# Optimization experiments

Measured on AMD Instinct MI355X. Metric: run time of the kernel, lower is better.

The kernel has to match this reference:

```python
import jax, jax.numpy as jnp
import numpy as np

N, E, IN, H, C = 50000, 800000, 128, 256, 2
EPS = 1e-5


def setup_inputs() -> dict:
    key = jax.random.key(0)
    ks = jax.random.split(key, 12)
    inp = {
        "x": jax.random.normal(ks[0], (N, IN), jnp.float32),
        "edge_index": jax.random.randint(ks[1], (2, E), 0, N, jnp.int32),
        "w_nei0": jax.random.normal(ks[2], (IN, H), jnp.float32) * 0.05,
        "w_root0": jax.random.normal(ks[3], (IN, H), jnp.float32) * 0.05,
        "b0": jnp.zeros((H,), jnp.float32),
        "w_nei": jax.random.normal(ks[4], (2, H, H), jnp.float32) * 0.05,
        "w_root": jax.random.normal(ks[5], (2, H, H), jnp.float32) * 0.05,
        "b": jnp.zeros((2, H), jnp.float32),
        "bn_gamma": jnp.ones((3, H), jnp.float32),
        "bn_beta": jnp.zeros((3, H), jnp.float32),
        "bn_mean": jax.random.normal(ks[6], (3, H), jnp.float32) * 0.05,
        "bn_var": jnp.ones((3, H), jnp.float32),
        "w1": jax.random.normal(ks[7], (H, H // 2), jnp.float32) * 0.05,
        "b1": jnp.zeros((H // 2,), jnp.float32),
        "w2": jax.random.normal(ks[8], (H // 2, C), jnp.float32) * 0.05,
        "b2": jnp.zeros((C,), jnp.float32),
    }
    return inp


def _mean_aggregate(h, src, dst, inv_deg):
    # gather source-node features, scatter-sum to destinations, divide by degree
    agg = jax.ops.segment_sum(h[src], dst, num_segments=N)  # (N, d)
    return agg * inv_deg[:, None]


def _forward(x, edge_index, w_nei0, w_root0, b0, w_nei, w_root, b,
             bn_gamma, bn_beta, bn_mean, bn_var, w1, b1, w2, b2):
    src, dst = edge_index[0], edge_index[1]
    deg = jax.ops.segment_sum(jnp.ones((E,), x.dtype), dst, num_segments=N)
    inv_deg = 1.0 / jnp.maximum(deg, 1.0)

    h = x
    wn_list = [w_nei0, w_nei[0], w_nei[1]]
    wr_list = [w_root0, w_root[0], w_root[1]]
    bias_list = [b0, b[0], b[1]]
    for i in range(3):
        mean_nb = _mean_aggregate(h, src, dst, inv_deg)          # (N, d_in)
        h = mean_nb @ wn_list[i] + bias_list[i] + h @ wr_list[i]  # SAGEConv
        # BatchNorm1d (eval: running stats) + ReLU; dropout is identity in eval
        h = (h - bn_mean[i]) * jax.lax.rsqrt(bn_var[i] + EPS) * bn_gamma[i] + bn_beta[i]
        h = jax.nn.relu(h)

    h = jax.nn.relu(h @ w1 + b1)
    logits = h @ w2 + b2
    return jax.nn.log_softmax(logits, axis=1)


def reference(x, edge_index, w_nei0, w_root0, b0, w_nei, w_root, b,
              bn_gamma, bn_beta, bn_mean, bn_var, w1, b1, w2, b2):
    return _forward(x, edge_index, w_nei0, w_root0, b0, w_nei, w_root, b,
                    bn_gamma, bn_beta, bn_mean, bn_var, w1, b1, w2, b2)
```

## Files before the change

kernel.cpp:

```cpp
#include <hip/hip_runtime.h>
#include <hip/hip_fp16.h>

#define N_NODES 50000
#define N_EDGES 800000
#define DIM_IN 128
#define DIM_H 256

typedef _Float16 f16;
typedef _Float16 half8 __attribute__((ext_vector_type(8)));
typedef _Float16 f16x4 __attribute__((ext_vector_type(4)));
typedef _Float16 f16x2 __attribute__((ext_vector_type(2)));
typedef float f32x4 __attribute__((ext_vector_type(4)));
typedef unsigned int u32;
typedef unsigned long long u64;

__device__ __forceinline__ void gload_lds16(const void* g, void* l) {
    __builtin_amdgcn_global_load_lds(
        (const __attribute__((address_space(1))) u32*)g,
        (__attribute__((address_space(3))) u32*)l,
        16, 0, 0);
}


__global__ void k_deg(const int* __restrict__ dst, int* __restrict__ deg) {
    int i = blockIdx.x * 256 + threadIdx.x;
    if (i < N_EDGES) atomicAdd(&deg[dst[i]], 1);
}

__global__ void k_scan1(const int* __restrict__ deg, int* __restrict__ row_start,
                        int* __restrict__ partials) {
    __shared__ int sm[256];
    int t = threadIdx.x;
    int i = blockIdx.x * 256 + t;
    int v = (i < N_NODES) ? deg[i] : 0;
    sm[t] = v;
    __syncthreads();
    for (int ofs = 1; ofs < 256; ofs <<= 1) {
        int add = (t >= ofs) ? sm[t - ofs] : 0;
        __syncthreads();
        sm[t] += add;
        __syncthreads();
    }
    if (i < N_NODES) row_start[i] = sm[t] - v;
    if (t == 255) partials[blockIdx.x] = sm[255];
}

__global__ void k_scan2(const int* __restrict__ partials, int* __restrict__ pscan, int nblk) {
    __shared__ int sm[256];
    int t = threadIdx.x;
    int v = (t < nblk) ? partials[t] : 0;
    sm[t] = v;
    __syncthreads();
    for (int ofs = 1; ofs < 256; ofs <<= 1) {
        int add = (t >= ofs) ? sm[t - ofs] : 0;
        __syncthreads();
        sm[t] += add;
        __syncthreads();
    }
    pscan[t] = sm[t] - v;
}

__global__ void k_scan3(const int* __restrict__ deg, int* __restrict__ row_start,
                        const int* __restrict__ pscan, float* __restrict__ inv_deg) {
    int i = blockIdx.x * 256 + threadIdx.x;
    if (i < N_NODES) {
        row_start[i] += pscan[blockIdx.x];
        int d = deg[i];
        inv_deg[i] = 1.0f / (float)(d > 1 ? d : 1);
        if (i == 0) row_start[N_NODES] = N_EDGES;
    }
}

__global__ void k_fill(const int* __restrict__ src, const int* __restrict__ dst,
                       const int* __restrict__ row_start, int* __restrict__ cursor,
                       int* __restrict__ csr) {
    int i = blockIdx.x * 256 + threadIdx.x;
    if (i < N_EDGES) {
        int d = dst[i];
        int p = atomicAdd(&cursor[d], 1);
        csr[row_start[d] + p] = src[i];
    }
}


__global__ void k_prep(const float* __restrict__ x, f16* __restrict__ hA,
                       const float* __restrict__ wn0, f16* __restrict__ Wn0t,
                       const float* __restrict__ wr0, f16* __restrict__ Wr0t,
                       const float* __restrict__ wn12, f16* __restrict__ Wn1t,
                       f16* __restrict__ Wn2t,
                       const float* __restrict__ wr12, f16* __restrict__ Wr1t,
                       f16* __restrict__ Wr2t,
                       const float* __restrict__ w1, f16* __restrict__ W1t,
                       const float* __restrict__ b0, const float* __restrict__ bvec,
                       const float* __restrict__ gamma, const float* __restrict__ beta,
                       const float* __restrict__ mean, const float* __restrict__ var,
                       const float* __restrict__ b1, float* __restrict__ st,
                       int* __restrict__ deg, int* __restrict__ cursor) {
    const int t = threadIdx.x;
    int b = blockIdx.x;
    auto tcvt = [&](const float* W, f16* Wt, int K, int NN, int bb) {
        int tt = bb * 256 + t;
        int n = tt / K, k = tt - n * K;
        Wt[tt] = (f16)W[(size_t)k * NN + n];
    };
    if (b < 391) {
        int i = b * 256 + t;
        if (i < N_NODES) deg[i] = 0;
        else if (i < 2 * N_NODES) cursor[i - N_NODES] = 0;
    } else if (b < 6641) {
        int i = (b - 391) * 256 + t;
        float4 v = ((const float4*)x)[i];
        f16x4 h = {(f16)v.x, (f16)v.y, (f16)v.z, (f16)v.w};
        *(f16x4*)(hA + (size_t)i * 4) = h;
    } else if (b < 6769) {
        tcvt(wn0, Wn0t, 128, 256, b - 6641);
    } else if (b < 6897) {
        tcvt(wr0, Wr0t, 128, 256, b - 6769);
    } else if (b < 7153) {
        tcvt(wn12, Wn1t, 256, 256, b - 6897);
    } else if (b < 7409) {
        tcvt(wn12 + 65536, Wn2t, 256, 256, b - 7153);
    } else if (b < 7665) {
        tcvt(wr12, Wr1t, 256, 256, b - 7409);
    } else if (b < 7921) {
        tcvt(wr12 + 65536, Wr2t, 256, 256, b - 7665);
    } else if (b < 8049) {
        tcvt(w1, W1t, 256, 128, b - 7921);
    } else {
        int c = t;
        for (int layer = 0; layer < 3; layer++) {
            float bias = (layer == 0) ? b0[c] : bvec[(layer - 1) * DIM_H + c];
            float g = gamma[layer * DIM_H + c];
            float be = beta[layer * DIM_H + c];
            float mu = mean[layer * DIM_H + c];
            float va = var[layer * DIM_H + c];
            float s = g * rsqrtf(va + 1e-5f);
            st[layer * 512 + c] = s;
            st[layer * 512 + 256 + c] = (bias - mu) * s + be;
        }
        st[3 * 512 + c] = 1.0f;
        st[3 * 512 + 256 + c] = (c < 128) ? b1[c] : 0.0f;
    }
}


template <int D>
__global__ void k_agg(const f16* __restrict__ h, const int* __restrict__ row_start,
                      const int* __restrict__ csr, const float* __restrict__ inv_deg,
                      f16* __restrict__ agg) {
    constexpr int V = D / 64;
    typedef _Float16 fvec __attribute__((ext_vector_type(V)));
    int wid = threadIdx.x >> 6;
    int lane = threadIdx.x & 63;
    int v = blockIdx.x * 4 + wid;
    if (v >= N_NODES) return;
    int e0 = row_start[v], e1 = row_start[v + 1];
    float acc[V];
#pragma unroll
    for (int j = 0; j < V; j++) acc[j] = 0.0f;

    const int li = lane & 15;
    for (int e = e0; e < e1; e += 16) {
        int ee = e + li;
        int idx = __builtin_nontemporal_load(&csr[ee < e1 ? ee : e1 - 1]);
        int rem = e1 - e;
        fvec hv[16];
#pragma unroll
        for (int j = 0; j < 16; j++) {
            int s = __shfl(idx, j);
            hv[j] = *(const fvec*)(h + (size_t)s * D + lane * V);
        }
#pragma unroll
        for (int j = 0; j < 16; j++) {
            if (j < rem) {
#pragma unroll
                for (int q = 0; q < V; q++) acc[q] += (float)hv[j][q];
            }
        }
    }

    float sc = inv_deg[v];
    fvec o;
#pragma unroll
    for (int j = 0; j < V; j++) o[j] = (f16)(acc[j] * sc);
    if constexpr (V == 2) {
        u32 raw; __builtin_memcpy(&raw, &o, 4);
        __builtin_nontemporal_store(raw, (u32*)(agg + (size_t)v * D + lane * V));
    } else {
        u64 raw; __builtin_memcpy(&raw, &o, 8);
        __builtin_nontemporal_store(raw, (u64*)(agg + (size_t)v * D + lane * V));
    }
}


__global__ __launch_bounds__(256) void k_gemm(
    const f16* __restrict__ A1, int lda1, const f16* __restrict__ B1, int k1,
    const f16* __restrict__ A2, int lda2, const f16* __restrict__ B2, int k2,
    const float* __restrict__ sc, const float* __restrict__ sh,
    f16* __restrict__ out, int ldo, int M) {
    __shared__ f16 aT[2][64 * 32];
    __shared__ f16 bT[2][256 * 32];
    const int tid = threadIdx.x;
    const int lane = tid & 63;
    const int wid = tid >> 6;
    const int m0 = blockIdx.x * 64;
    f32x4 acc[4][4] = {};

    const int srow = tid >> 2;
    const int schunk = (tid & 3) ^ ((tid >> 3) & 3);
    const int ktot = k1 + k2;

    auto stage = [&](int buf, int kk) {
        const f16 *Ap, *Bp;
        int lda, ldb, kloc;
        if (kk < k1) { Ap = A1; Bp = B1; lda = lda1; ldb = k1; kloc = kk; }
        else         { Ap = A2; Bp = B2; lda = lda2; ldb = k2; kloc = kk - k1; }
        int gm = m0 + srow;
        gm = gm < M ? gm : M - 1;
        gload_lds16(Ap + (size_t)gm * lda + kloc + schunk * 8,
                    (char*)&aT[buf][0] + tid * 16);
#pragma unroll
        for (int hh = 0; hh < 4; hh++) {
            gload_lds16(Bp + (size_t)(hh * 64 + srow) * ldb + kloc + schunk * 8,
                        (char*)&bT[buf][0] + hh * 4096 + tid * 16);
        }
    };

    auto compute = [&](int buf) {
        half8 af[4], bf[4];
#pragma unroll
        for (int mi = 0; mi < 4; mi++) {
            int row = mi * 16 + (lane & 15);
            int ch = (lane >> 4) ^ ((row >> 1) & 3);
            af[mi] = *(const half8*)((const char*)&aT[buf][0] + row * 64 + ch * 16);
        }
#pragma unroll
        for (int ni = 0; ni < 4; ni++) {
            int row = wid * 64 + ni * 16 + (lane & 15);
            int ch = (lane >> 4) ^ ((row >> 1) & 3);
            bf[ni] = *(const half8*)((const char*)&bT[buf][0] + row * 64 + ch * 16);
        }
#pragma unroll
        for (int mi = 0; mi < 4; mi++)
#pragma unroll
            for (int ni = 0; ni < 4; ni++)
                acc[mi][ni] = __builtin_amdgcn_mfma_f32_16x16x32_f16(af[mi], bf[ni],
                                                                     acc[mi][ni], 0, 0, 0);
    };

    stage(0, 0);
    __syncthreads();
    int cur = 0;
    for (int kk = 32; kk < ktot; kk += 32) {
        stage(cur ^ 1, kk);
        compute(cur);
        __syncthreads();
        cur ^= 1;
    }
    compute(cur);

#pragma unroll
    for (int mi = 0; mi < 4; mi++) {
#pragma unroll
        for (int ni = 0; ni < 4; ni++) {
            int gcol = wid * 64 + ni * 16 + (lane & 15);
            float s = sc[gcol], t = sh[gcol];
#pragma unroll
            for (int r = 0; r < 4; r++) {
                int grow = m0 + mi * 16 + (lane >> 4) * 4 + r;
                if (grow < M) {
                    float val = fmaxf(acc[mi][ni][r] * s + t, 0.0f);
                    out[(size_t)grow * ldo + gcol] = (f16)val;
                }
            }
        }
    }
}


__global__ __launch_bounds__(256) void k_gemm_head(
    const f16* __restrict__ A1, int k1, const f16* __restrict__ B1,
    const float* __restrict__ sh,
    const float* __restrict__ w2, const float* __restrict__ b2,
    float* __restrict__ out, int M) {
    __shared__ f16 aT[2][128 * 32];
    __shared__ f16 bT[2][128 * 32];
    __shared__ float smred[128][2][2];
    const int tid = threadIdx.x;
    const int lane = tid & 63;
    const int wid = tid >> 6;
    const int wm = wid >> 1, wn = wid & 1;
    const int m0 = blockIdx.x * 128;
    f32x4 acc[4][4] = {};

    const int srow = tid >> 2;
    const int schunk = (tid & 3) ^ ((tid >> 3) & 3);

    auto stage = [&](int buf, int kk) {
#pragma unroll
        for (int hh = 0; hh < 2; hh++) {
            int r = hh * 64 + srow;
            int gm = m0 + r;
            gm = gm < M ? gm : M - 1;
            gload_lds16(A1 + (size_t)gm * k1 + kk + schunk * 8,
                        (char*)&aT[buf][0] + hh * 4096 + tid * 16);
            gload_lds16(B1 + (size_t)r * k1 + kk + schunk * 8,
                        (char*)&bT[buf][0] + hh * 4096 + tid * 16);
        }
    };

    auto compute = [&](int buf) {
        half8 af[4], bf[4];
#pragma unroll
        for (int mi = 0; mi < 4; mi++) {
            int row = wm * 64 + mi * 16 + (lane & 15);
            int ch = (lane >> 4) ^ ((row >> 1) & 3);
            af[mi] = *(const half8*)((const char*)&aT[buf][0] + row * 64 + ch * 16);
        }
#pragma unroll
        for (int ni = 0; ni < 4; ni++) {
            int row = wn * 64 + ni * 16 + (lane & 15);
            int ch = (lane >> 4) ^ ((row >> 1) & 3);
            bf[ni] = *(const half8*)((const char*)&bT[buf][0] + row * 64 + ch * 16);
        }
#pragma unroll
        for (int mi = 0; mi < 4; mi++)
#pragma unroll
            for (int ni = 0; ni < 4; ni++)
                acc[mi][ni] = __builtin_amdgcn_mfma_f32_16x16x32_f16(af[mi], bf[ni],
                                                                     acc[mi][ni], 0, 0, 0);
    };

    stage(0, 0);
    __syncthreads();
    int cur = 0;
    for (int kk = 32; kk < k1; kk += 32) {
        stage(cur ^ 1, kk);
        compute(cur);
        __syncthreads();
        cur ^= 1;
    }
    compute(cur);

    float w2c[4][2], shc[4];
#pragma unroll
    for (int ni = 0; ni < 4; ni++) {
        int c = wn * 64 + ni * 16 + (lane & 15);
        w2c[ni][0] = w2[c * 2];
        w2c[ni][1] = w2[c * 2 + 1];
        shc[ni] = sh[c];
    }
#pragma unroll
    for (int mi = 0; mi < 4; mi++) {
#pragma unroll
        for (int r = 0; r < 4; r++) {
            float p0 = 0.0f, p1 = 0.0f;
#pragma unroll
            for (int ni = 0; ni < 4; ni++) {
                float val = fmaxf(acc[mi][ni][r] + shc[ni], 0.0f);
                p0 += val * w2c[ni][0];
                p1 += val * w2c[ni][1];
            }
#pragma unroll
            for (int o = 1; o < 16; o <<= 1) {
                p0 += __shfl_xor(p0, o);
                p1 += __shfl_xor(p1, o);
            }
            if ((lane & 15) == 0) {
                int lrow = wm * 64 + mi * 16 + (lane >> 4) * 4 + r;
                smred[lrow][wn][0] = p0;
                smred[lrow][wn][1] = p1;
            }
        }
    }
    __syncthreads();
    if (tid < 128) {
        int grow = m0 + tid;
        if (grow < M) {
            float l0 = smred[tid][0][0] + smred[tid][1][0] + b2[0];
            float l1 = smred[tid][0][1] + smred[tid][1][1] + b2[1];
            float m = fmaxf(l0, l1);
            float lse = m + logf(expf(l0 - m) + expf(l1 - m));
            out[(size_t)grow * 2] = l0 - lse;
            out[(size_t)grow * 2 + 1] = l1 - lse;
        }
    }
}


extern "C" void kernel_launch(void* const* d_in, const int* in_sizes, int n_in,
                              void* d_out, int out_size, void* d_ws, size_t ws_size,
                              hipStream_t stream) {
    const float* x     = (const float*)d_in[0];
    const int*   ei    = (const int*)d_in[1];
    const float* wn0   = (const float*)d_in[2];
    const float* wr0   = (const float*)d_in[3];
    const float* b0    = (const float*)d_in[4];
    const float* wn12  = (const float*)d_in[5];
    const float* wr12  = (const float*)d_in[6];
    const float* bvec  = (const float*)d_in[7];
    const float* gamma = (const float*)d_in[8];
    const float* beta  = (const float*)d_in[9];
    const float* mean  = (const float*)d_in[10];
    const float* var   = (const float*)d_in[11];
    const float* w1    = (const float*)d_in[12];
    const float* b1    = (const float*)d_in[13];
    const float* w2    = (const float*)d_in[14];
    const float* b2    = (const float*)d_in[15];
    const int* srcv = ei;
    const int* dstv = ei + N_EDGES;

    char* p = (char*)d_ws;
    auto alloc = [&](size_t bytes) {
        char* r = p;
        p += (bytes + 255) & ~(size_t)255;
        return r;
    };
    int*   deg       = (int*)alloc((size_t)N_NODES * 4);
    int*   row_start = (int*)alloc((size_t)(N_NODES + 1) * 4);
    int*   cursor    = (int*)alloc((size_t)N_NODES * 4);
    float* inv_deg   = (float*)alloc((size_t)N_NODES * 4);
    int*   partials  = (int*)alloc(256 * 4);
    int*   pscan     = (int*)alloc(256 * 4);
    int*   csr       = (int*)alloc((size_t)N_EDGES * 4);
    f16*   Wn0t      = (f16*)alloc(128 * 256 * 2);
    f16*   Wr0t      = (f16*)alloc(128 * 256 * 2);
    f16*   Wn1t      = (f16*)alloc(256 * 256 * 2);
    f16*   Wr1t      = (f16*)alloc(256 * 256 * 2);
    f16*   Wn2t      = (f16*)alloc(256 * 256 * 2);
    f16*   Wr2t      = (f16*)alloc(256 * 256 * 2);
    f16*   W1t       = (f16*)alloc(256 * 128 * 2);
    float* st        = (float*)alloc(4 * 512 * 4);
    f16*   hA        = (f16*)alloc((size_t)N_NODES * 256 * 2);
    f16*   hB        = (f16*)alloc((size_t)N_NODES * 256 * 2);
    f16*   agg       = (f16*)alloc((size_t)N_NODES * 256 * 2);

    const int EB = (N_EDGES + 255) / 256;
    const int NBLK = (N_NODES + 255) / 256;

    k_prep<<<8050, 256, 0, stream>>>(x, hA, wn0, Wn0t, wr0, Wr0t,
                                     wn12, Wn1t, Wn2t, wr12, Wr1t, Wr2t,
                                     w1, W1t, b0, bvec, gamma, beta, mean, var,
                                     b1, st, deg, cursor);
    k_deg<<<EB, 256, 0, stream>>>(dstv, deg);
    k_scan1<<<NBLK, 256, 0, stream>>>(deg, row_start, partials);
    k_scan2<<<1, 256, 0, stream>>>(partials, pscan, NBLK);
    k_scan3<<<NBLK, 256, 0, stream>>>(deg, row_start, pscan, inv_deg);
    k_fill<<<EB, 256, 0, stream>>>(srcv, dstv, row_start, cursor, csr);

    const int AB = (N_NODES + 3) / 4;
    const int GB = (N_NODES + 63) / 64;

    k_agg<128><<<AB, 256, 0, stream>>>(hA, row_start, csr, inv_deg, agg);
    k_gemm<<<GB, 256, 0, stream>>>(agg, 128, Wn0t, 128, hA, 128, Wr0t, 128,
                                   st + 0, st + 256, hB, 256, N_NODES);
    k_agg<256><<<AB, 256, 0, stream>>>(hB, row_start, csr, inv_deg, agg);
    k_gemm<<<GB, 256, 0, stream>>>(agg, 256, Wn1t, 256, hB, 256, Wr1t, 256,
                                   st + 512, st + 768, hA, 256, N_NODES);
    k_agg<256><<<AB, 256, 0, stream>>>(hA, row_start, csr, inv_deg, agg);
    k_gemm<<<GB, 256, 0, stream>>>(agg, 256, Wn2t, 256, hA, 256, Wr2t, 256,
                                   st + 1024, st + 1280, hB, 256, N_NODES);
    k_gemm_head<<<(N_NODES + 127) / 128, 256, 0, stream>>>(
        hB, 256, W1t, st + 1792, w2, b2, (float*)d_out, N_NODES);
}
```

Measured before the change: 357.1 us.

## Overlap root-weight GEMM with neighbor aggregation in one launch; fold degree count into prep

Each layer's root-path GEMM (h @ Wr) now runs in the same launch as the neighbor gather and aggregation, using separate block ranges. The aim is to overlap compute-bound MFMA work with the memory-bound gather. The neighbor GEMM then adds the stored f16 root partial before applying BN and ReLU. The degree atomic-count kernel is merged into the prep kernel, and zero-initialisation moves to memsets. In exchange, the root partial is rounded to f16 and makes an extra round trip through global memory each layer, and aggregation stores lose their nontemporal hints.

```diff
diff --git a/kernel.cpp b/kernel.cpp
--- a/kernel.cpp
+++ b/kernel.cpp
@@ -12,7 +12,6 @@
 typedef _Float16 f16x2 __attribute__((ext_vector_type(2)));
 typedef float f32x4 __attribute__((ext_vector_type(4)));
 typedef unsigned int u32;
-typedef unsigned long long u64;
 
 __device__ __forceinline__ void gload_lds16(const void* g, void* l) {
     __builtin_amdgcn_global_load_lds(
@@ -21,11 +20,6 @@
         16, 0, 0);
 }
 
-
-__global__ void k_deg(const int* __restrict__ dst, int* __restrict__ deg) {
-    int i = blockIdx.x * 256 + threadIdx.x;
-    if (i < N_EDGES) atomicAdd(&deg[dst[i]], 1);
-}
 
 __global__ void k_scan1(const int* __restrict__ deg, int* __restrict__ row_start,
                         int* __restrict__ partials) {
@@ -95,7 +89,7 @@
                        const float* __restrict__ gamma, const float* __restrict__ beta,
                        const float* __restrict__ mean, const float* __restrict__ var,
                        const float* __restrict__ b1, float* __restrict__ st,
-                       int* __restrict__ deg, int* __restrict__ cursor) {
+                       const int* __restrict__ dst, int* __restrict__ deg) {
     const int t = threadIdx.x;
     int b = blockIdx.x;
     auto tcvt = [&](const float* W, f16* Wt, int K, int NN, int bb) {
@@ -103,30 +97,26 @@
         int n = tt / K, k = tt - n * K;
         Wt[tt] = (f16)W[(size_t)k * NN + n];
     };
-    if (b < 391) {
+    if (b < 6250) {
         int i = b * 256 + t;
-        if (i < N_NODES) deg[i] = 0;
-        else if (i < 2 * N_NODES) cursor[i - N_NODES] = 0;
-    } else if (b < 6641) {
-        int i = (b - 391) * 256 + t;
         float4 v = ((const float4*)x)[i];
         f16x4 h = {(f16)v.x, (f16)v.y, (f16)v.z, (f16)v.w};
         *(f16x4*)(hA + (size_t)i * 4) = h;
-    } else if (b < 6769) {
-        tcvt(wn0, Wn0t, 128, 256, b - 6641);
-    } else if (b < 6897) {
-        tcvt(wr0, Wr0t, 128, 256, b - 6769);
-    } else if (b < 7153) {
-        tcvt(wn12, Wn1t, 256, 256, b - 6897);
-    } else if (b < 7409) {
-        tcvt(wn12 + 65536, Wn2t, 256, 256, b - 7153);
-    } else if (b < 7665) {
-        tcvt(wr12, Wr1t, 256, 256, b - 7409);
-    } else if (b < 7921) {
-        tcvt(wr12 + 65536, Wr2t, 256, 256, b - 7665);
-    } else if (b < 8049) {
-        tcvt(w1, W1t, 256, 128, b - 7921);
-    } else {
+    } else if (b < 6378) {
+        tcvt(wn0, Wn0t, 128, 256, b - 6250);
+    } else if (b < 6506) {
+        tcvt(wr0, Wr0t, 128, 256, b - 6378);
+    } else if (b < 6762) {
+        tcvt(wn12, Wn1t, 256, 256, b - 6506);
+    } else if (b < 7018) {
+        tcvt(wn12 + 65536, Wn2t, 256, 256, b - 6762);
+    } else if (b < 7274) {
+        tcvt(wr12, Wr1t, 256, 256, b - 7018);
+    } else if (b < 7530) {
+        tcvt(wr12 + 65536, Wr2t, 256, 256, b - 7274);
+    } else if (b < 7658) {
+        tcvt(w1, W1t, 256, 128, b - 7530);
+    } else if (b == 7658) {
         int c = t;
         for (int layer = 0; layer < 3; layer++) {
             float bias = (layer == 0) ? b0[c] : bvec[(layer - 1) * DIM_H + c];
@@ -140,64 +130,134 @@
         }
         st[3 * 512 + c] = 1.0f;
         st[3 * 512 + 256 + c] = (c < 128) ? b1[c] : 0.0f;
+    } else {
+        int i = (b - 7659) * 256 + t;
+        if (i < N_EDGES) atomicAdd(&deg[dst[i]], 1);
     }
 }
 
 
 template <int D>
-__global__ void k_agg(const f16* __restrict__ h, const int* __restrict__ row_start,
-                      const int* __restrict__ csr, const float* __restrict__ inv_deg,
-                      f16* __restrict__ agg) {
-    constexpr int V = D / 64;
-    typedef _Float16 fvec __attribute__((ext_vector_type(V)));
-    int wid = threadIdx.x >> 6;
-    int lane = threadIdx.x & 63;
-    int v = blockIdx.x * 4 + wid;
-    if (v >= N_NODES) return;
-    int e0 = row_start[v], e1 = row_start[v + 1];
-    float acc[V];
-#pragma unroll
-    for (int j = 0; j < V; j++) acc[j] = 0.0f;
-
-    const int li = lane & 15;
-    for (int e = e0; e < e1; e += 16) {
-        int ee = e + li;
-        int idx = __builtin_nontemporal_load(&csr[ee < e1 ? ee : e1 - 1]);
-        int rem = e1 - e;
-        fvec hv[16];
-#pragma unroll
-        for (int j = 0; j < 16; j++) {
-            int s = __shfl(idx, j);
-            hv[j] = *(const fvec*)(h + (size_t)s * D + lane * V);
-        }
-#pragma unroll
-        for (int j = 0; j < 16; j++) {
-            if (j < rem) {
-#pragma unroll
-                for (int q = 0; q < V; q++) acc[q] += (float)hv[j][q];
-            }
-        }
-    }
-
-    float sc = inv_deg[v];
-    fvec o;
-#pragma unroll
-    for (int j = 0; j < V; j++) o[j] = (f16)(acc[j] * sc);
-    if constexpr (V == 2) {
-        u32 raw; __builtin_memcpy(&raw, &o, 4);
-        __builtin_nontemporal_store(raw, (u32*)(agg + (size_t)v * D + lane * V));
+__global__ __launch_bounds__(256) void k_fused(
+    const f16* __restrict__ h, const int* __restrict__ row_start,
+    const int* __restrict__ csr, const float* __restrict__ inv_deg,
+    f16* __restrict__ agg,
+    const f16* __restrict__ Wr,
+    f16* __restrict__ Croot,
+    int ngemm) {
+    __shared__ f16 aT[2][64 * 32];
+    __shared__ f16 bT[2][256 * 32];
+    const int tid = threadIdx.x;
+    const int lane = tid & 63;
+    const int wid = tid >> 6;
+
+    if ((int)blockIdx.x < ngemm) {
+        const int m0 = blockIdx.x * 64;
+        f32x4 acc[4][4] = {};
+        const int srow = tid >> 2;
+        const int schunk = (tid & 3) ^ ((tid >> 3) & 3);
+
+        auto stage = [&](int buf, int kk) {
+            int gm = m0 + srow;
+            gm = gm < N_NODES ? gm : N_NODES - 1;
+            gload_lds16(h + (size_t)gm * D + kk + schunk * 8,
+                        (char*)&aT[buf][0] + tid * 16);
+#pragma unroll
+            for (int hh = 0; hh < 4; hh++) {
+                gload_lds16(Wr + (size_t)(hh * 64 + srow) * D + kk + schunk * 8,
+                            (char*)&bT[buf][0] + hh * 4096 + tid * 16);
+            }
+        };
+        auto compute = [&](int buf) {
+            half8 af[4], bf[4];
+#pragma unroll
+            for (int mi = 0; mi < 4; mi++) {
+                int row = mi * 16 + (lane & 15);
+                int ch = (lane >> 4) ^ ((row >> 1) & 3);
+                af[mi] = *(const half8*)((const char*)&aT[buf][0] + row * 64 + ch * 16);
+            }
+#pragma unroll
+            for (int ni = 0; ni < 4; ni++) {
+                int row = wid * 64 + ni * 16 + (lane & 15);
+                int ch = (lane >> 4) ^ ((row >> 1) & 3);
+                bf[ni] = *(const half8*)((const char*)&bT[buf][0] + row * 64 + ch * 16);
+            }
+#pragma unroll
+            for (int mi = 0; mi < 4; mi++)
+#pragma unroll
+                for (int ni = 0; ni < 4; ni++)
+                    acc[mi][ni] = __builtin_amdgcn_mfma_f32_16x16x32_f16(af[mi], bf[ni],
+                                                                         acc[mi][ni], 0, 0, 0);
+        };
+
+        stage(0, 0);
+        __syncthreads();
+        int cur = 0;
+        for (int kk = 32; kk < D; kk += 32) {
+            stage(cur ^ 1, kk);
+            compute(cur);
+            __syncthreads();
+            cur ^= 1;
+        }
+        compute(cur);
+
+#pragma unroll
+        for (int mi = 0; mi < 4; mi++) {
+#pragma unroll
+            for (int ni = 0; ni < 4; ni++) {
+                int gcol = wid * 64 + ni * 16 + (lane & 15);
+#pragma unroll
+                for (int r = 0; r < 4; r++) {
+                    int grow = m0 + mi * 16 + (lane >> 4) * 4 + r;
+                    if (grow < N_NODES)
+                        Croot[(size_t)grow * 256 + gcol] = (f16)acc[mi][ni][r];
+                }
+            }
+        }
     } else {
-        u64 raw; __builtin_memcpy(&raw, &o, 8);
-        __builtin_nontemporal_store(raw, (u64*)(agg + (size_t)v * D + lane * V));
-    }
-}
-
-
-__global__ __launch_bounds__(256) void k_gemm(
-    const f16* __restrict__ A1, int lda1, const f16* __restrict__ B1, int k1,
-    const f16* __restrict__ A2, int lda2, const f16* __restrict__ B2, int k2,
+        constexpr int V = D / 64;
+        typedef _Float16 fvec __attribute__((ext_vector_type(V)));
+        int v = (blockIdx.x - ngemm) * 4 + wid;
+        if (v >= N_NODES) return;
+        int e0 = row_start[v], e1 = row_start[v + 1];
+        float acc[V];
+#pragma unroll
+        for (int j = 0; j < V; j++) acc[j] = 0.0f;
+
+        const int li = lane & 15;
+        for (int e = e0; e < e1; e += 16) {
+            int ee = e + li;
+            int idx = csr[ee < e1 ? ee : e1 - 1];
+            int rem = e1 - e;
+            fvec hv[16];
+#pragma unroll
+            for (int j = 0; j < 16; j++) {
+                int s = __shfl(idx, j);
+                hv[j] = *(const fvec*)(h + (size_t)s * D + lane * V);
+            }
+#pragma unroll
+            for (int j = 0; j < 16; j++) {
+                if (j < rem) {
+#pragma unroll
+                    for (int q = 0; q < V; q++) acc[q] += (float)hv[j][q];
+                }
+            }
+        }
+
+        float sc = inv_deg[v];
+        fvec o;
+#pragma unroll
+        for (int j = 0; j < V; j++) o[j] = (f16)(acc[j] * sc);
+        *(fvec*)(agg + (size_t)v * D + lane * V) = o;
+    }
+}
+
+
+__global__ __launch_bounds__(256) void k_gemm_nei(
+    const f16* __restrict__ A1, int k1, const f16* __restrict__ B1,
+    const f16* Croot,
     const float* __restrict__ sc, const float* __restrict__ sh,
-    f16* __restrict__ out, int ldo, int M) {
+    f16* out, int M) {
     __shared__ f16 aT[2][64 * 32];
     __shared__ f16 bT[2][256 * 32];
     const int tid = threadIdx.x;
@@ -208,24 +268,18 @@
 
     const int srow = tid >> 2;
     const int schunk = (tid & 3) ^ ((tid >> 3) & 3);
-    const int ktot = k1 + k2;
 
     auto stage = [&](int buf, int kk) {
-        const f16 *Ap, *Bp;
-        int lda, ldb, kloc;
-        if (kk < k1) { Ap = A1; Bp = B1; lda = lda1; ldb = k1; kloc = kk; }
-        else         { Ap = A2; Bp = B2; lda = lda2; ldb = k2; kloc = kk - k1; }
         int gm = m0 + srow;
         gm = gm < M ? gm : M - 1;
-        gload_lds16(Ap + (size_t)gm * lda + kloc + schunk * 8,
+        gload_lds16(A1 + (size_t)gm * k1 + kk + schunk * 8,
                     (char*)&aT[buf][0] + tid * 16);
 #pragma unroll
         for (int hh = 0; hh < 4; hh++) {
-            gload_lds16(Bp + (size_t)(hh * 64 + srow) * ldb + kloc + schunk * 8,
+            gload_lds16(B1 + (size_t)(hh * 64 + srow) * k1 + kk + schunk * 8,
                         (char*)&bT[buf][0] + hh * 4096 + tid * 16);
         }
     };
-
     auto compute = [&](int buf) {
         half8 af[4], bf[4];
 #pragma unroll
@@ -251,7 +305,7 @@
     stage(0, 0);
     __syncthreads();
     int cur = 0;
-    for (int kk = 32; kk < ktot; kk += 32) {
+    for (int kk = 32; kk < k1; kk += 32) {
         stage(cur ^ 1, kk);
         compute(cur);
         __syncthreads();
@@ -269,8 +323,9 @@
             for (int r = 0; r < 4; r++) {
                 int grow = m0 + mi * 16 + (lane >> 4) * 4 + r;
                 if (grow < M) {
-                    float val = fmaxf(acc[mi][ni][r] * s + t, 0.0f);
-                    out[(size_t)grow * ldo + gcol] = (f16)val;
+                    float cr = (float)Croot[(size_t)grow * 256 + gcol];
+                    float val = fmaxf((acc[mi][ni][r] + cr) * s + t, 0.0f);
+                    out[(size_t)grow * 256 + gcol] = (f16)val;
                 }
             }
         }
@@ -435,14 +490,16 @@
     f16*   hB        = (f16*)alloc((size_t)N_NODES * 256 * 2);
     f16*   agg       = (f16*)alloc((size_t)N_NODES * 256 * 2);
 
+    hipMemsetAsync(deg, 0, (size_t)N_NODES * 4, stream);
+    hipMemsetAsync(cursor, 0, (size_t)N_NODES * 4, stream);
+
     const int EB = (N_EDGES + 255) / 256;
     const int NBLK = (N_NODES + 255) / 256;
 
-    k_prep<<<8050, 256, 0, stream>>>(x, hA, wn0, Wn0t, wr0, Wr0t,
-                                     wn12, Wn1t, Wn2t, wr12, Wr1t, Wr2t,
-                                     w1, W1t, b0, bvec, gamma, beta, mean, var,
-                                     b1, st, deg, cursor);
-    k_deg<<<EB, 256, 0, stream>>>(dstv, deg);
+    k_prep<<<10784, 256, 0, stream>>>(x, hA, wn0, Wn0t, wr0, Wr0t,
+                                      wn12, Wn1t, Wn2t, wr12, Wr1t, Wr2t,
+                                      w1, W1t, b0, bvec, gamma, beta, mean, var,
+                                      b1, st, dstv, deg);
     k_scan1<<<NBLK, 256, 0, stream>>>(deg, row_start, partials);
     k_scan2<<<1, 256, 0, stream>>>(partials, pscan, NBLK);
     k_scan3<<<NBLK, 256, 0, stream>>>(deg, row_start, pscan, inv_deg);
@@ -451,15 +508,18 @@
     const int AB = (N_NODES + 3) / 4;
     const int GB = (N_NODES + 63) / 64;
 
-    k_agg<128><<<AB, 256, 0, stream>>>(hA, row_start, csr, inv_deg, agg);
-    k_gemm<<<GB, 256, 0, stream>>>(agg, 128, Wn0t, 128, hA, 128, Wr0t, 128,
-                                   st + 0, st + 256, hB, 256, N_NODES);
-    k_agg<256><<<AB, 256, 0, stream>>>(hB, row_start, csr, inv_deg, agg);
-    k_gemm<<<GB, 256, 0, stream>>>(agg, 256, Wn1t, 256, hB, 256, Wr1t, 256,
-                                   st + 512, st + 768, hA, 256, N_NODES);
-    k_agg<256><<<AB, 256, 0, stream>>>(hA, row_start, csr, inv_deg, agg);
-    k_gemm<<<GB, 256, 0, stream>>>(agg, 256, Wn2t, 256, hA, 256, Wr2t, 256,
-                                   st + 1024, st + 1280, hB, 256, N_NODES);
+    k_fused<128><<<GB + AB, 256, 0, stream>>>(hA, row_start, csr, inv_deg, agg,
+                                              Wr0t, hB, GB);
+    k_gemm_nei<<<GB, 256, 0, stream>>>(agg, 128, Wn0t, hB, st + 0, st + 256,
+                                       hB, N_NODES);
+    k_fused<256><<<GB + AB, 256, 0, stream>>>(hB, row_start, csr, inv_deg, agg,
+                                              Wr1t, hA, GB);
+    k_gemm_nei<<<GB, 256, 0, stream>>>(agg, 256, Wn1t, hA, st + 512, st + 768,
+                                       hA, N_NODES);
+    k_fused<256><<<GB + AB, 256, 0, stream>>>(hA, row_start, csr, inv_deg, agg,
+                                              Wr2t, hB, GB);
+    k_gemm_nei<<<GB, 256, 0, stream>>>(agg, 256, Wn2t, hB, st + 1024, st + 1280,
+                                       hB, N_NODES);
     k_gemm_head<<<(N_NODES + 127) / 128, 256, 0, stream>>>(
         hB, 256, W1t, st + 1792, w2, b2, (float*)d_out, N_NODES);
 }
```

Result: slower. 530.5 us (+48.6%).
